# Kernel optimization log

Hardware: AMD Instinct MI355X
Metric: run time of the kernel (lower is better)

Reference implementation:

```python
import jax, jax.numpy as jnp
import numpy as np

N_NODES = 100000
N_EDGES = 1000000
D = 64
HID = 64
OUT = 64
N_CLS = 10
N_GRAPHS = 512
BN_EPS = 1e-5


def setup_inputs() -> dict:
    key = jax.random.key(0)
    ks = jax.random.split(key, 16)
    inp = {
        "x": jax.random.normal(ks[0], (N_NODES, D), dtype=jnp.float32),
        "edge_index": jax.random.randint(ks[1], (2, N_EDGES), 0, N_NODES, dtype=jnp.int32),
        "batch": jnp.sort(jax.random.randint(ks[2], (N_NODES,), 0, N_GRAPHS, dtype=jnp.int32)),
    }
    def lin(k, fi, fo):
        lim = 1.0 / np.sqrt(fi)
        kw, kb = jax.random.split(k)
        return (jax.random.uniform(kw, (fi, fo), minval=-lim, maxval=lim, dtype=jnp.float32),
                jax.random.uniform(kb, (fo,), minval=-lim, maxval=lim, dtype=jnp.float32))
    # conv0 MLP([64,64,64]) with BN after first linear
    inp["w0a"], inp["b0a"] = lin(ks[3], D, HID)
    inp["g0"] = jnp.ones((HID,), jnp.float32); inp["be0"] = jnp.zeros((HID,), jnp.float32)
    inp["m0"] = jnp.zeros((HID,), jnp.float32); inp["v0"] = jnp.ones((HID,), jnp.float32)
    inp["w0b"], inp["b0b"] = lin(ks[4], HID, HID)
    # conv1 MLP([64,64,64])
    inp["w1a"], inp["b1a"] = lin(ks[5], HID, HID)
    inp["g1"] = jnp.ones((HID,), jnp.float32); inp["be1"] = jnp.zeros((HID,), jnp.float32)
    inp["m1"] = jnp.zeros((HID,), jnp.float32); inp["v1"] = jnp.ones((HID,), jnp.float32)
    inp["w1b"], inp["b1b"] = lin(ks[6], HID, OUT)
    # classifier
    inp["wc"], inp["bc"] = lin(ks[7], OUT, N_CLS)
    return inp


def _bn_eval(h, g, b, m, v):
    return (h - m) * jax.lax.rsqrt(v + BN_EPS) * g + b


def _mlp(h, wa, ba, g, be, m, v, wb, bb):
    # Linear -> BN -> ReLU -> (dropout eval=identity) -> Linear
    h = h @ wa + ba
    h = jax.nn.relu(_bn_eval(h, g, be, m, v))
    return h @ wb + bb


def _gin_conv(h, src, dst, wa, ba, g, be, m, v, wb, bb):
    # GINConv eps=0: mlp(x + sum_{j->i} x_j), messages scatter-added at dst
    agg = jax.ops.segment_sum(h[src], dst, num_segments=N_NODES)
    return _mlp(h + agg, wa, ba, g, be, m, v, wb, bb)


def reference(x, edge_index, batch,
              w0a, b0a, g0, be0, m0, v0, w0b, b0b,
              w1a, b1a, g1, be1, m1, v1, w1b, b1b,
              wc, bc):
    src, dst = edge_index[0], edge_index[1]
    h = _gin_conv(x, src, dst, w0a, b0a, g0, be0, m0, v0, w0b, b0b)
    h = jax.nn.relu(h)  # dropout is identity in eval
    h = _gin_conv(h, src, dst, w1a, b1a, g1, be1, m1, v1, w1b, b1b)
    # global mean pool over batch indices
    sums = jax.ops.segment_sum(h, batch, num_segments=N_GRAPHS)
    cnts = jax.ops.segment_sum(jnp.ones((h.shape[0],), h.dtype), batch, num_segments=N_GRAPHS)
    pooled = sums / jnp.maximum(cnts, 1.0)[:, None]
    return pooled @ wc + bc
```

## Files before the change

### kernel.cpp

```cpp
#include <hip/hip_runtime.h>

#define N_NODES 100000
#define N_EDGES 1000000
#define N_GRAPHS 512
#define N_CLS 10
#define BN_EPS 1e-5f

#define SCAN_NB 200
#define NTILES2 3125

typedef _Float16 half8 __attribute__((ext_vector_type(8)));
typedef _Float16 half4v __attribute__((ext_vector_type(4)));
typedef float floatx4 __attribute__((ext_vector_type(4)));

__global__ __launch_bounds__(256) void prep_kernel(
    const float* __restrict__ x, _Float16* __restrict__ xh,
    const int* __restrict__ batch, const int* __restrict__ dstI,
    int* __restrict__ deg, int* __restrict__ rank,
    const float* __restrict__ w0a, const float* __restrict__ b0a,
    const float* __restrict__ g0, const float* __restrict__ be0,
    const float* __restrict__ m0, const float* __restrict__ v0,
    const float* __restrict__ w0b,
    const float* __restrict__ w1a, const float* __restrict__ b1a,
    const float* __restrict__ g1, const float* __restrict__ be1,
    const float* __restrict__ m1, const float* __restrict__ v1,
    const float* __restrict__ w1b,
    int* __restrict__ gstart,
    _Float16* __restrict__ wHi, _Float16* __restrict__ wLo,
    float* __restrict__ b1p0, float* __restrict__ b1p1) {
    const int gid = blockIdx.x * 256 + threadIdx.x;

    if (gid < 1600000) {
        float4 v = ((const float4*)x)[gid];
        half4v h = {(_Float16)v.x, (_Float16)v.y, (_Float16)v.z, (_Float16)v.w};
        ((half4v*)xh)[gid] = h;
    }

    if (gid < N_EDGES)
        rank[gid] = atomicAdd(&deg[dstI[gid]], 1);

    if (gid <= N_NODES) {
        int bcur = (gid < N_NODES) ? batch[gid] : N_GRAPHS;
        int bprev = (gid > 0) ? batch[gid - 1] : -1;
        for (int g = bprev + 1; g <= bcur; ++g) gstart[g] = gid;
    }

    if (gid < 16384) {
        const int e = gid & 4095, mat = gid >> 12;
        const int jj = e & 7, lane = (e >> 3) & 63, c = (e >> 9) & 3, k0 = (e >> 11) & 1;
        const int k = k0 * 32 + (lane >> 4) * 8 + jj;
        const int col = c * 16 + (lane & 15);
        float val;
        if (mat == 0)      val = w0a[k * 64 + col] * (rsqrtf(v0[col] + BN_EPS) * g0[col]);
        else if (mat == 1) val = w0b[k * 64 + col];
        else if (mat == 2) val = w1a[k * 64 + col] * (rsqrtf(v1[col] + BN_EPS) * g1[col]);
        else               val = w1b[k * 64 + col];
        _Float16 hi = (_Float16)val;
        wHi[gid] = hi;
        wLo[gid] = (_Float16)(val - (float)hi);
    }

    if (gid >= 16384 && gid < 16512) {
        int t = gid - 16384;
        if (t < 64) {
            float s = rsqrtf(v0[t] + BN_EPS) * g0[t];
            b1p0[t] = (b0a[t] - m0[t]) * s + be0[t];
        } else {
            t -= 64;
            float s = rsqrtf(v1[t] + BN_EPS) * g1[t];
            b1p1[t] = (b1a[t] - m1[t]) * s + be1[t];
        }
    }
}

__global__ __launch_bounds__(256) void scanA_kernel(const int* __restrict__ deg,
                                                    int* __restrict__ bsum) {
    __shared__ int sh[256];
    const int base = blockIdx.x * 512;
    const int t = threadIdx.x;
    int a = 0, b = 0;
    if (base + t < N_NODES) a = deg[base + t];
    if (base + 256 + t < N_NODES) b = deg[base + 256 + t];
    sh[t] = a + b;
    __syncthreads();
#pragma unroll
    for (int off = 128; off > 0; off >>= 1) {
        if (t < off) sh[t] += sh[t + off];
        __syncthreads();
    }
    if (t == 0) bsum[blockIdx.x] = sh[0];
}

__global__ __launch_bounds__(256) void scanC_kernel(const int* __restrict__ deg,
                                                    const int* __restrict__ bsum,
                                                    int* __restrict__ rowptr) {
    __shared__ int sh[256];
    __shared__ int sboff[256];
    const int base = blockIdx.x * 512;
    const int t = threadIdx.x;

    const int bv = (t < SCAN_NB) ? bsum[t] : 0;
    sboff[t] = bv;

    const int i0 = base + 2 * t, i1 = i0 + 1;
    const int d0 = (i0 < N_NODES) ? deg[i0] : 0;
    const int d1 = (i1 < N_NODES) ? deg[i1] : 0;
    const int p = d0 + d1;
    sh[t] = p;
    __syncthreads();
#pragma unroll
    for (int off = 1; off < 256; off <<= 1) {
        int u = (t >= off) ? sh[t - off] : 0;
        int ub = (t >= off) ? sboff[t - off] : 0;
        __syncthreads();
        sh[t] += u;
        sboff[t] += ub;
        __syncthreads();
    }
    const int myoff = (blockIdx.x == 0) ? 0 : sboff[blockIdx.x - 1];
    const int excl = myoff + sh[t] - p;
    if (i0 < N_NODES) rowptr[i0] = excl;
    if (i1 < N_NODES) rowptr[i1] = excl + d0;
    if (blockIdx.x == 0 && t == 0) rowptr[N_NODES] = N_EDGES;
}

__global__ __launch_bounds__(256) void fill_kernel(const int* __restrict__ srcI,
                                                   const int* __restrict__ dstI,
                                                   const int* __restrict__ rank,
                                                   const int* __restrict__ rowptr,
                                                   int* __restrict__ sortedSrc) {
    int e = blockIdx.x * 256 + threadIdx.x;
    if (e >= N_EDGES) return;
    sortedSrc[rowptr[dstI[e]] + rank[e]] = srcI[e];
}

template <int POOL>
__global__ __launch_bounds__(128) void conv_mfma(
    const _Float16* __restrict__ in, const int* __restrict__ rowptr,
    const int* __restrict__ srcList,
    const _Float16* __restrict__ wH1, const _Float16* __restrict__ wL1,
    const _Float16* __restrict__ wH2, const _Float16* __restrict__ wL2,
    const float* __restrict__ b1, const float* __restrict__ b2,
    _Float16* __restrict__ out, const int* __restrict__ batch,
    float* __restrict__ pooled) {
    __shared__ __align__(16) _Float16 scratch[2][2304];
    __shared__ float pooledLoc[8 * 64];
    __shared__ int bIds[32];
    __shared__ int maxSlot;

    const int tid = threadIdx.x;
    const int j = tid & 63, wv = tid >> 6;
    const int eoff = j >> 4;
    const int lf = j & 15;
    const int base = blockIdx.x * 32;
    const int strip0 = base + wv * 16;

    if (POOL) {
#pragma unroll
        for (int q = 0; q < 4; ++q) pooledLoc[tid + q * 128] = 0.f;
        if (tid == 0) maxSlot = 0;
        if (j < 16) bIds[wv * 16 + j] = batch[strip0 + j];
    }

    const int rpv = rowptr[strip0 + min(j, 16)];

    _Float16* aggH = scratch[wv];
    _Float16* aggL = scratch[wv] + 1152;

    for (int mq = 0; mq < 4; ++mq) {
        const int m0 = mq * 4;
        int rr[5];
#pragma unroll
        for (int i = 0; i < 5; ++i) rr[i] = __builtin_amdgcn_readlane(rpv, m0 + i);
        int cnt[4];
#pragma unroll
        for (int i = 0; i < 4; ++i) cnt[i] = rr[i + 1] - rr[i];

        float aR[4][4];
#pragma unroll
        for (int i = 0; i < 4; ++i)
#pragma unroll
            for (int q = 0; q < 4; ++q) aR[i][q] = 0.f;

        half4v sS[4];
#pragma unroll
        for (int i = 0; i < 4; ++i) {
            sS[i] = (half4v){0, 0, 0, 0};
            if (eoff == 0)
                sS[i] = *(const half4v*)(in + (size_t)(strip0 + m0 + i) * 64 + lf * 4);
        }
        half4v vT[4][4];
#pragma unroll
        for (int i = 0; i < 4; ++i) {
            const int g = (min(cnt[i], 16) + 3) >> 2;
#pragma unroll
            for (int k = 0; k < 4; ++k) {
                vT[i][k] = (half4v){0, 0, 0, 0};
                if (k < g) {
                    int ec = min(4 * k + eoff, cnt[i] - 1);
                    int id = srcList[rr[i] + ec];
                    vT[i][k] = *(const half4v*)(in + (size_t)id * 64 + lf * 4);
                }
            }
        }
#pragma unroll
        for (int i = 0; i < 4; ++i) {
#pragma unroll
            for (int k = 0; k < 4; ++k) {
                if (4 * k + eoff < cnt[i]) {
                    aR[i][0] += (float)vT[i][k].x; aR[i][1] += (float)vT[i][k].y;
                    aR[i][2] += (float)vT[i][k].z; aR[i][3] += (float)vT[i][k].w;
                }
            }
        }
#pragma unroll
        for (int i = 0; i < 4; ++i) {
            for (int eb = 16; eb < cnt[i]; eb += 16) {
#pragma unroll
                for (int k = 0; k < 4; ++k) {
                    int e_ = eb + 4 * k + eoff;
                    if (e_ < cnt[i]) {
                        int id = srcList[rr[i] + e_];
                        half4v t = *(const half4v*)(in + (size_t)id * 64 + lf * 4);
                        aR[i][0] += (float)t.x; aR[i][1] += (float)t.y;
                        aR[i][2] += (float)t.z; aR[i][3] += (float)t.w;
                    }
                }
            }
        }
#pragma unroll
        for (int i = 0; i < 4; ++i) {
            if (eoff == 0) {
                aR[i][0] += (float)sS[i].x; aR[i][1] += (float)sS[i].y;
                aR[i][2] += (float)sS[i].z; aR[i][3] += (float)sS[i].w;
            }
#pragma unroll
            for (int q = 0; q < 4; ++q) {
                aR[i][q] += __shfl_xor(aR[i][q], 16, 64);
                aR[i][q] += __shfl_xor(aR[i][q], 32, 64);
            }
            if (j < 16) {
                half4v hi, lo;
#pragma unroll
                for (int q = 0; q < 4; ++q) {
                    hi[q] = (_Float16)aR[i][q];
                    lo[q] = (_Float16)(aR[i][q] - (float)hi[q]);
                }
                *(half4v*)(aggH + (m0 + i) * 72 + 4 * j) = hi;
                *(half4v*)(aggL + (m0 + i) * 72 + 4 * j) = lo;
            }
        }
    }

    const int l15 = j & 15, quad = j >> 4;
    const floatx4 vzero = {0.f, 0.f, 0.f, 0.f};

    floatx4 acc[4] = {vzero, vzero, vzero, vzero};
    {
        const _Float16* aH0 = aggH + l15 * 72 + quad * 8;
        const _Float16* aL0 = aggL + l15 * 72 + quad * 8;
#pragma unroll
        for (int k0 = 0; k0 < 2; ++k0) {
            half8 aH = *(const half8*)(aH0 + k0 * 32);
            half8 aL = *(const half8*)(aL0 + k0 * 32);
#pragma unroll
            for (int c = 0; c < 4; ++c) {
                const int fo = ((k0 * 4 + c) * 64 + j) * 8;
                half8 bH = *(const half8*)(wH1 + fo);
                half8 bL = *(const half8*)(wL1 + fo);
                acc[c] = __builtin_amdgcn_mfma_f32_16x16x32_f16(aH, bH, acc[c], 0, 0, 0);
                acc[c] = __builtin_amdgcn_mfma_f32_16x16x32_f16(aL, bH, acc[c], 0, 0, 0);
                acc[c] = __builtin_amdgcn_mfma_f32_16x16x32_f16(aH, bL, acc[c], 0, 0, 0);
            }
        }
    }
    _Float16* hH = aggH;
    _Float16* hL = aggL;
#pragma unroll
    for (int c = 0; c < 4; ++c) {
        const float bv = b1[c * 16 + l15];
#pragma unroll
        for (int r = 0; r < 4; ++r) {
            const int row = quad * 4 + r, col = c * 16 + l15;
            float v = acc[c][r] + bv;
            v = fmaxf(v, 0.f);
            const _Float16 hi = (_Float16)v;
            hH[row * 72 + col] = hi;
            hL[row * 72 + col] = (_Float16)(v - (float)hi);
        }
    }

    floatx4 acc2[4] = {vzero, vzero, vzero, vzero};
    {
        const _Float16* aH0 = hH + l15 * 72 + quad * 8;
        const _Float16* aL0 = hL + l15 * 72 + quad * 8;
#pragma unroll
        for (int k0 = 0; k0 < 2; ++k0) {
            half8 aH = *(const half8*)(aH0 + k0 * 32);
            half8 aL = *(const half8*)(aL0 + k0 * 32);
#pragma unroll
            for (int c = 0; c < 4; ++c) {
                const int fo = ((k0 * 4 + c) * 64 + j) * 8;
                half8 bH = *(const half8*)(wH2 + fo);
                half8 bL = *(const half8*)(wL2 + fo);
                acc2[c] = __builtin_amdgcn_mfma_f32_16x16x32_f16(aH, bH, acc2[c], 0, 0, 0);
                acc2[c] = __builtin_amdgcn_mfma_f32_16x16x32_f16(aL, bH, acc2[c], 0, 0, 0);
                acc2[c] = __builtin_amdgcn_mfma_f32_16x16x32_f16(aH, bL, acc2[c], 0, 0, 0);
            }
        }
    }

    if (!POOL) {
#pragma unroll
        for (int c = 0; c < 4; ++c) {
            const float bv = b2[c * 16 + l15];
#pragma unroll
            for (int r = 0; r < 4; ++r) {
                const int node = strip0 + quad * 4 + r;
                out[(size_t)node * 64 + c * 16 + l15] =
                    (_Float16)fmaxf(acc2[c][r] + bv, 0.f);
            }
        }
    } else {
        float* oT = (float*)scratch[wv];
#pragma unroll
        for (int c = 0; c < 4; ++c) {
            const float bv = b2[c * 16 + l15];
#pragma unroll
            for (int r = 0; r < 4; ++r)
                oT[(quad * 4 + r) * 66 + c * 16 + l15] = acc2[c][r] + bv;
        }
        __syncthreads();
        const int b0 = bIds[0];
        int curB = -1;
        float accv = 0.f;
        for (int r = 0; r < 16; ++r) {
            const int b = bIds[wv * 16 + r];
            const float v = oT[r * 66 + j];
            if (b != curB) {
                if (curB >= 0) {
                    const int s = curB - b0;
                    if (s >= 0 && s < 8) {
                        atomicAdd(&pooledLoc[s * 64 + j], accv);
                        if (j == 0) atomicMax(&maxSlot, s);
                    } else {
                        atomicAdd(&pooled[curB * 64 + j], accv);
                    }
                }
                curB = b;
                accv = v;
            } else {
                accv += v;
            }
        }
        {
            const int s = curB - b0;
            if (s >= 0 && s < 8) {
                atomicAdd(&pooledLoc[s * 64 + j], accv);
                if (j == 0) atomicMax(&maxSlot, s);
            } else {
                atomicAdd(&pooled[curB * 64 + j], accv);
            }
        }
        __syncthreads();
        const int ns = maxSlot + 1;
        for (int s = wv; s < ns; s += 2)
            atomicAdd(&pooled[(b0 + s) * 64 + j], pooledLoc[s * 64 + j]);
    }
}

__global__ __launch_bounds__(64) void classifier_kernel(const float* __restrict__ pooled,
                                                        const int* __restrict__ gstart,
                                                        const float* __restrict__ wc,
                                                        const float* __restrict__ bc,
                                                        float* __restrict__ out) {
    const int g = blockIdx.x;
    const int j = threadIdx.x;
    const float c = fmaxf((float)(gstart[g + 1] - gstart[g]), 1.f);
    const float mean = pooled[g * 64 + j] / c;
#pragma unroll
    for (int cc = 0; cc < N_CLS; ++cc) {
        float p = mean * wc[j * N_CLS + cc];
#pragma unroll
        for (int off = 32; off > 0; off >>= 1) p += __shfl_down(p, off, 64);
        if (j == 0) out[g * N_CLS + cc] = p + bc[cc];
    }
}


extern "C" void kernel_launch(void* const* d_in, const int* in_sizes, int n_in,
                              void* d_out, int out_size, void* d_ws, size_t ws_size,
                              hipStream_t stream) {
    const float* x   = (const float*)d_in[0];
    const int*   ei  = (const int*)d_in[1];
    const int* batch = (const int*)d_in[2];
    const float* w0a = (const float*)d_in[3];
    const float* b0a = (const float*)d_in[4];
    const float* g0  = (const float*)d_in[5];
    const float* be0 = (const float*)d_in[6];
    const float* m0  = (const float*)d_in[7];
    const float* v0  = (const float*)d_in[8];
    const float* w0b = (const float*)d_in[9];
    const float* b0b = (const float*)d_in[10];
    const float* w1a = (const float*)d_in[11];
    const float* b1a = (const float*)d_in[12];
    const float* g1  = (const float*)d_in[13];
    const float* be1 = (const float*)d_in[14];
    const float* m1  = (const float*)d_in[15];
    const float* v1  = (const float*)d_in[16];
    const float* w1b = (const float*)d_in[17];
    const float* b1b = (const float*)d_in[18];
    const float* wc  = (const float*)d_in[19];
    const float* bc  = (const float*)d_in[20];
    float* out = (float*)d_out;

    const int* srcI = ei;
    const int* dstI = ei + N_EDGES;

    int* ws = (int*)d_ws;
    int*      deg       = ws;
    int*      bsum      = ws + 100000;
    float*    pooled    = (float*)(ws + 100404);
    int*      rowptr    = ws + 133172;
    int*      rank      = ws + 233176;
    int*      sortedSrc = ws + 1233176;
    _Float16* xh        = (_Float16*)(ws + 2233176);
    _Float16* h1        = (_Float16*)(ws + 5433176);
    float*    b1p0      = (float*)(ws + 8633176);
    float*    b1p1      = (float*)(ws + 8633240);
    int*      gstart    = ws + 8633304;
    _Float16* wHi       = (_Float16*)(ws + 8633820);
    _Float16* wLo       = (_Float16*)(ws + 8642012);

    (void)hipMemsetAsync((void*)deg, 0, 133172 * sizeof(int), stream);
    prep_kernel<<<6250, 256, 0, stream>>>(x, xh, batch, dstI, deg, rank,
                                          w0a, b0a, g0, be0, m0, v0, w0b,
                                          w1a, b1a, g1, be1, m1, v1, w1b,
                                          gstart, wHi, wLo, b1p0, b1p1);

    scanA_kernel<<<SCAN_NB, 256, 0, stream>>>(deg, bsum);
    scanC_kernel<<<SCAN_NB, 256, 0, stream>>>(deg, bsum, rowptr);
    fill_kernel<<<(N_EDGES + 255) / 256, 256, 0, stream>>>(srcI, dstI, rank, rowptr, sortedSrc);

    conv_mfma<0><<<NTILES2, 128, 0, stream>>>(xh, rowptr, sortedSrc,
                                              wHi, wLo, wHi + 4096, wLo + 4096,
                                              b1p0, b0b, h1, nullptr, nullptr);

    conv_mfma<1><<<NTILES2, 128, 0, stream>>>(h1, rowptr, sortedSrc,
                                              wHi + 8192, wLo + 8192, wHi + 12288, wLo + 12288,
                                              b1p1, b1b, nullptr, batch, pooled);

    classifier_kernel<<<N_GRAPHS, 64, 0, stream>>>(pooled, gstart, wc, bc, out);
}
```

Before: 296.6 us.

## Software-pipeline neighbor index and row gathers across node groups in conv kernel

```diff
diff --git a/kernel.cpp b/kernel.cpp
--- a/kernel.cpp
+++ b/kernel.cpp
@@ -134,8 +134,101 @@
     sortedSrc[rowptr[dstI[e]] + rank[e]] = srcI[e];
 }
 
+__device__ __forceinline__ void idx_stage(const int* __restrict__ srcList, int rpv,
+                                          int mq, int nodeSel, int slotSel, int& idxOwn) {
+    const int rr0 = __shfl(rpv, mq * 4 + nodeSel, 64);
+    const int rr1 = __shfl(rpv, mq * 4 + nodeSel + 1, 64);
+    const int c = rr1 - rr0;
+    const int e0 = (c > 0) ? min(slotSel, c - 1) : 0;
+    int pos = rr0 + e0;
+    pos = min(pos, N_EDGES - 1);
+    idxOwn = srcList[pos];
+}
+
+__device__ __forceinline__ void rows_stage(const _Float16* __restrict__ in, int rpv,
+                                           int mq, int strip0, int eoff, int lf,
+                                           int idxOwn, half4v (&vT)[4][4], half4v (&sS)[4]) {
+    const int m0 = mq * 4;
+#pragma unroll
+    for (int i = 0; i < 4; ++i) {
+        sS[i] = (half4v){0, 0, 0, 0};
+        if (eoff == 0)
+            sS[i] = *(const half4v*)(in + (size_t)(strip0 + m0 + i) * 64 + lf * 4);
+    }
+#pragma unroll
+    for (int i = 0; i < 4; ++i) {
+        const int rr0 = __builtin_amdgcn_readlane(rpv, m0 + i);
+        const int rr1 = __builtin_amdgcn_readlane(rpv, m0 + i + 1);
+        const int cI = rr1 - rr0;
+        const int g = (min(cI, 16) + 3) >> 2;
+#pragma unroll
+        for (int k = 0; k < 4; ++k) {
+            vT[i][k] = (half4v){0, 0, 0, 0};
+            if (k < g) {
+                const int id = __shfl(idxOwn, i * 16 + 4 * k + eoff, 64);
+                vT[i][k] = *(const half4v*)(in + (size_t)id * 64 + lf * 4);
+            }
+        }
+    }
+}
+
+__device__ __forceinline__ void consume_stage(const _Float16* __restrict__ in,
+                                              const int* __restrict__ srcList, int rpv,
+                                              int mq, int eoff, int lf, int j,
+                                              const half4v (&vT)[4][4], const half4v (&sS)[4],
+                                              _Float16* aggH, _Float16* aggL) {
+    const int m0 = mq * 4;
+#pragma unroll
+    for (int i = 0; i < 4; ++i) {
+        const int rr0 = __builtin_amdgcn_readlane(rpv, m0 + i);
+        const int rr1 = __builtin_amdgcn_readlane(rpv, m0 + i + 1);
+        const int cI = rr1 - rr0;
+        float aR[4] = {0.f, 0.f, 0.f, 0.f};
+#pragma unroll
+        for (int k = 0; k < 4; ++k) {
+            if (4 * k + eoff < cI) {
+                aR[0] += (float)vT[i][k].x; aR[1] += (float)vT[i][k].y;
+                aR[2] += (float)vT[i][k].z; aR[3] += (float)vT[i][k].w;
+            }
+        }
+        for (int eb = 16; eb < cI; eb += 16) {
+#pragma unroll
+            for (int k = 0; k < 4; ++k) {
+                const int e_ = eb + 4 * k + eoff;
+                if (e_ < cI) {
+                    const int id = srcList[rr0 + e_];
+                    half4v t = *(const half4v*)(in + (size_t)id * 64 + lf * 4);
+                    aR[0] += (float)t.x; aR[1] += (float)t.y;
+                    aR[2] += (float)t.z; aR[3] += (float)t.w;
+                }
+            }
+        }
+        if (eoff == 0) {
+            aR[0] += (float)sS[i].x; aR[1] += (float)sS[i].y;
+            aR[2] += (float)sS[i].z; aR[3] += (float)sS[i].w;
+        }
+#pragma unroll
+        for (int q = 0; q < 4; ++q) {
+            aR[q] += __shfl_xor(aR[q], 16, 64);
+            aR[q] += __shfl_xor(aR[q], 32, 64);
+        }
+        if (j < 16) {
+            half4v hi, lo;
+#pragma unroll
+            for (int q = 0; q < 4; ++q) {
+                hi[q] = (_Float16)aR[q];
+                lo[q] = (_Float16)(aR[q] - (float)hi[q]);
+            }
+            *(half4v*)(aggH + (m0 + i) * 72 + 4 * j) = hi;
+            *(half4v*)(aggL + (m0 + i) * 72 + 4 * j) = lo;
+        }
+    }
+}
+
+#define SBAR() __builtin_amdgcn_sched_barrier(0)
+
 template <int POOL>
-__global__ __launch_bounds__(128) void conv_mfma(
+__global__ __launch_bounds__(128, 4) void conv_mfma(
     const _Float16* __restrict__ in, const int* __restrict__ rowptr,
     const int* __restrict__ srcList,
     const _Float16* __restrict__ wH1, const _Float16* __restrict__ wL1,
@@ -167,89 +260,32 @@
     _Float16* aggH = scratch[wv];
     _Float16* aggL = scratch[wv] + 1152;
 
-    for (int mq = 0; mq < 4; ++mq) {
-        const int m0 = mq * 4;
-        int rr[5];
-#pragma unroll
-        for (int i = 0; i < 5; ++i) rr[i] = __builtin_amdgcn_readlane(rpv, m0 + i);
-        int cnt[4];
-#pragma unroll
-        for (int i = 0; i < 4; ++i) cnt[i] = rr[i + 1] - rr[i];
-
-        float aR[4][4];
-#pragma unroll
-        for (int i = 0; i < 4; ++i)
-#pragma unroll
-            for (int q = 0; q < 4; ++q) aR[i][q] = 0.f;
-
-        half4v sS[4];
-#pragma unroll
-        for (int i = 0; i < 4; ++i) {
-            sS[i] = (half4v){0, 0, 0, 0};
-            if (eoff == 0)
-                sS[i] = *(const half4v*)(in + (size_t)(strip0 + m0 + i) * 64 + lf * 4);
-        }
-        half4v vT[4][4];
-#pragma unroll
-        for (int i = 0; i < 4; ++i) {
-            const int g = (min(cnt[i], 16) + 3) >> 2;
-#pragma unroll
-            for (int k = 0; k < 4; ++k) {
-                vT[i][k] = (half4v){0, 0, 0, 0};
-                if (k < g) {
-                    int ec = min(4 * k + eoff, cnt[i] - 1);
-                    int id = srcList[rr[i] + ec];
-                    vT[i][k] = *(const half4v*)(in + (size_t)id * 64 + lf * 4);
-                }
-            }
-        }
-#pragma unroll
-        for (int i = 0; i < 4; ++i) {
-#pragma unroll
-            for (int k = 0; k < 4; ++k) {
-                if (4 * k + eoff < cnt[i]) {
-                    aR[i][0] += (float)vT[i][k].x; aR[i][1] += (float)vT[i][k].y;
-                    aR[i][2] += (float)vT[i][k].z; aR[i][3] += (float)vT[i][k].w;
-                }
-            }
-        }
-#pragma unroll
-        for (int i = 0; i < 4; ++i) {
-            for (int eb = 16; eb < cnt[i]; eb += 16) {
-#pragma unroll
-                for (int k = 0; k < 4; ++k) {
-                    int e_ = eb + 4 * k + eoff;
-                    if (e_ < cnt[i]) {
-                        int id = srcList[rr[i] + e_];
-                        half4v t = *(const half4v*)(in + (size_t)id * 64 + lf * 4);
-                        aR[i][0] += (float)t.x; aR[i][1] += (float)t.y;
-                        aR[i][2] += (float)t.z; aR[i][3] += (float)t.w;
-                    }
-                }
-            }
-        }
-#pragma unroll
-        for (int i = 0; i < 4; ++i) {
-            if (eoff == 0) {
-                aR[i][0] += (float)sS[i].x; aR[i][1] += (float)sS[i].y;
-                aR[i][2] += (float)sS[i].z; aR[i][3] += (float)sS[i].w;
-            }
-#pragma unroll
-            for (int q = 0; q < 4; ++q) {
-                aR[i][q] += __shfl_xor(aR[i][q], 16, 64);
-                aR[i][q] += __shfl_xor(aR[i][q], 32, 64);
-            }
-            if (j < 16) {
-                half4v hi, lo;
-#pragma unroll
-                for (int q = 0; q < 4; ++q) {
-                    hi[q] = (_Float16)aR[i][q];
-                    lo[q] = (_Float16)(aR[i][q] - (float)hi[q]);
-                }
-                *(half4v*)(aggH + (m0 + i) * 72 + 4 * j) = hi;
-                *(half4v*)(aggL + (m0 + i) * 72 + 4 * j) = lo;
-            }
-        }
+    {
+        int idxA, idxB, idxC;
+        half4v vA[4][4], vB[4][4], sA[4], sB[4];
+
+        idx_stage(srcList, rpv, 0, eoff, lf, idxA);
+        idx_stage(srcList, rpv, 1, eoff, lf, idxB);
+        SBAR();
+        rows_stage(in, rpv, 0, strip0, eoff, lf, idxA, vA, sA);
+        SBAR();
+        idx_stage(srcList, rpv, 2, eoff, lf, idxC);
+        SBAR();
+        rows_stage(in, rpv, 1, strip0, eoff, lf, idxB, vB, sB);
+        SBAR();
+        consume_stage(in, srcList, rpv, 0, eoff, lf, j, vA, sA, aggH, aggL);
+        SBAR();
+        idx_stage(srcList, rpv, 3, eoff, lf, idxA);
+        SBAR();
+        rows_stage(in, rpv, 2, strip0, eoff, lf, idxC, vA, sA);
+        SBAR();
+        consume_stage(in, srcList, rpv, 1, eoff, lf, j, vB, sB, aggH, aggL);
+        SBAR();
+        rows_stage(in, rpv, 3, strip0, eoff, lf, idxA, vB, sB);
+        SBAR();
+        consume_stage(in, srcList, rpv, 2, eoff, lf, j, vA, sA, aggH, aggL);
+        SBAR();
+        consume_stage(in, srcList, rpv, 3, eoff, lf, j, vB, sB, aggH, aggL);
     }
 
     const int l15 = j & 15, quad = j >> 4;
```

Measured after the change: 279.1 us. 5.9% less time.
